# Kernel tuning notes

Hardware: AMD Instinct MI355X
Metric: run time of the kernel (lower is better)

Reference implementation:

```python
import jax, jax.numpy as jnp
import numpy as np
import math

PHI = (1.0 + math.sqrt(5.0)) / 2.0
LN_EPS = 1e-5


def _carrier_phases(n_heads: int) -> np.ndarray:
    """Reproduce DimensionalHeadManager._allocate carrier phases."""
    base = [k * math.pi / 7.0 for k in range(7)]  # rung base phases
    n_rungs = 7
    raw = []
    remaining = n_heads
    for i in range(n_rungs):
        if i < n_rungs - 1:
            c = max(1, round(n_heads / PHI ** (i + 1)))
            c = min(c, remaining - (n_rungs - 1 - i))
            raw.append(c)
            remaining -= c
        else:
            raw.append(max(1, remaining))
    phases = []
    for rung_idx, count in enumerate(raw):
        for j in range(count):
            phases.append(base[rung_idx] + 2.0 * math.pi / max(count, 1) * j)
    return np.asarray(phases[:n_heads], dtype=np.float32)


def setup_inputs() -> dict:
    key = jax.random.key(0)
    ks = jax.random.split(key, 7)
    B, S, D, H = 2, 2048, 1024, 16
    w_scale = 0.02  # realistic init scale for Linear weights
    x = jax.random.normal(ks[0], (B, S, D), dtype=jnp.float32)
    Wq = jax.random.normal(ks[1], (D, D), dtype=jnp.float32) * w_scale
    Wk = jax.random.normal(ks[2], (D, D), dtype=jnp.float32) * w_scale
    Wv = jax.random.normal(ks[3], (D, D), dtype=jnp.float32) * w_scale
    Wo = jax.random.normal(ks[4], (D, D), dtype=jnp.float32) * w_scale
    Wp = jax.random.normal(ks[5], (D,), dtype=jnp.float32) * w_scale  # W_phase (1,D) flattened
    gamma = jnp.ones((D,), dtype=jnp.float32)
    beta = jnp.zeros((D,), dtype=jnp.float32)
    carrier = jnp.asarray(_carrier_phases(H))  # srl.carrier_freq init
    lam = jnp.float32(0.1)  # lambda_resonance init
    return {"x": x, "Wq": Wq, "Wk": Wk, "Wv": Wv, "Wo": Wo, "Wp": Wp,
            "gamma": gamma, "beta": beta, "carrier": carrier, "lam": lam}


def reference(x, Wq, Wk, Wv, Wo, Wp, gamma, beta, carrier, lam):
    B, S, D = x.shape
    H = carrier.shape[0]
    dh = D // H
    scale = 1.0 / math.sqrt(dh)

    residual = x
    # LayerNorm
    mu = jnp.mean(x, axis=-1, keepdims=True)
    var = jnp.mean((x - mu) ** 2, axis=-1, keepdims=True)
    xn = (x - mu) * jax.lax.rsqrt(var + LN_EPS) * gamma + beta

    # Q/K/V projections (torch Linear: y = x @ W.T), split into heads
    q = jnp.einsum('bsd,ed->bse', xn, Wq).reshape(B, S, H, dh)
    k = jnp.einsum('bsd,ed->bse', xn, Wk).reshape(B, S, H, dh)
    v = jnp.einsum('bsd,ed->bse', xn, Wv).reshape(B, S, H, dh)

    # scalar phase per token, per-head carrier resonance gate
    phase = jnp.einsum('bsd,d->bs', xn, Wp)                       # (B,S)
    head_T = jnp.cos((phase[..., None] - carrier) * 0.5) ** 2     # (B,S,H)

    # attention scores + resonance term R_ij = cos^2((phi_i - phi_j)/2)
    scores = jnp.einsum('bihd,bjhd->bhij', q, k) * scale          # (B,H,S,S)
    R = jnp.cos((phase[:, :, None] - phase[:, None, :]) * 0.5) ** 2  # (B,S,S)
    scores = scores + lam * R[:, None, :, :]

    attn = jax.nn.softmax(scores, axis=-1)
    out = jnp.einsum('bhij,bjhd->bihd', attn, v)                  # (B,S,H,dh)
    out = out * head_T[..., None]                                 # per-head resonance gating
    emergent_energy = jnp.sum(jnp.abs(out))
    y = residual + jnp.einsum('bse,de->bsd', out.reshape(B, S, D), Wo)
    return (y, emergent_energy)
```

## Files before the change

kernel.cpp:

```cpp
#include <hip/hip_runtime.h>
#include <hip/hip_bf16.h>

#define S_LEN 2048
#define D_MODEL 1024
#define NH 16
#define DH 64
#define M_TOK 4096
#define DK 80

typedef __attribute__((ext_vector_type(8))) short bf16x8;
typedef __attribute__((ext_vector_type(4))) float f32x4;
typedef __attribute__((ext_vector_type(16))) float f32x16;

#define LOG2E 1.4426950408889634f

__device__ __forceinline__ unsigned short f2bf(float f) {
  unsigned u = __float_as_uint(f);
  u += 0x7FFF + ((u >> 16) & 1);
  return (unsigned short)(u >> 16);
}

__device__ __forceinline__ void gl16(const void* g, void* l) {
  __builtin_amdgcn_global_load_lds(
      (const __attribute__((address_space(1))) unsigned int*)g,
      (__attribute__((address_space(3))) unsigned int*)l, 16, 0, 0);
}

__global__ __launch_bounds__(256) void prep_kernel(
    const float* __restrict__ Wq, const float* __restrict__ Wk,
    const float* __restrict__ Wv, const float* __restrict__ Wo,
    unsigned short* __restrict__ wbf, float* __restrict__ energy) {
  if (blockIdx.x == 0 && threadIdx.x == 0) *energy = 0.f;
  int idx = (blockIdx.x * 256 + threadIdx.x) * 4;
  int wsel = idx >> 20;
  const float* s = (wsel == 0) ? Wq : (wsel == 1) ? Wk : (wsel == 2) ? Wv : Wo;
  int off = idx & 1048575;
  float4 v = *(const float4*)(s + off);
  ushort4 p;
  p.x = f2bf(v.x); p.y = f2bf(v.y); p.z = f2bf(v.z); p.w = f2bf(v.w);
  *(ushort4*)(wbf + idx) = p;
}

__device__ __forceinline__ float block_sum(float v, float* sm) {
#pragma unroll
  for (int o = 32; o > 0; o >>= 1) v += __shfl_xor(v, o, 64);
  int w = threadIdx.x >> 6;
  __syncthreads();
  if ((threadIdx.x & 63) == 0) sm[w] = v;
  __syncthreads();
  return sm[0] + sm[1] + sm[2] + sm[3];
}

__global__ __launch_bounds__(256) void ln_phase_kernel(
    const float* __restrict__ x, const float* __restrict__ Wp,
    const float* __restrict__ gamma, const float* __restrict__ beta,
    unsigned short* __restrict__ xn, float* __restrict__ cosP,
    float* __restrict__ sinP) {
  __shared__ float sm[4];
  int row = blockIdx.x;
  int tid = threadIdx.x;
  float4 v = ((const float4*)(x + (size_t)row * D_MODEL))[tid];
  float mu = block_sum(v.x + v.y + v.z + v.w, sm) * (1.0f / D_MODEL);
  float d0 = v.x - mu, d1 = v.y - mu, d2 = v.z - mu, d3 = v.w - mu;
  float var = block_sum(d0 * d0 + d1 * d1 + d2 * d2 + d3 * d3, sm) * (1.0f / D_MODEL);
  float rinv = rsqrtf(var + 1e-5f);
  float4 g = ((const float4*)gamma)[tid];
  float4 be = ((const float4*)beta)[tid];
  float n0 = d0 * rinv * g.x + be.x;
  float n1 = d1 * rinv * g.y + be.y;
  float n2 = d2 * rinv * g.z + be.z;
  float n3 = d3 * rinv * g.w + be.w;
  ushort4 p;
  p.x = f2bf(n0); p.y = f2bf(n1); p.z = f2bf(n2); p.w = f2bf(n3);
  ((ushort4*)(xn + (size_t)row * D_MODEL))[tid] = p;
  float4 wp = ((const float4*)Wp)[tid];
  float ph = block_sum(n0 * wp.x + n1 * wp.y + n2 * wp.z + n3 * wp.w, sm);
  if (tid == 0) {
    cosP[row] = cosf(ph);
    sinP[row] = sinf(ph);
  }
}

__global__ __launch_bounds__(256) void phase_fill_kernel(
    const float* __restrict__ cosP, const float* __restrict__ sinP,
    unsigned short* __restrict__ kk80) {
  int gid = blockIdx.x * 256 + threadIdx.x;
  int s = gid & (S_LEN - 1);
  int bh = gid >> 11;
  int b = bh >> 4;
  int tok = b * S_LEN + s;
  unsigned int w0 = (unsigned int)f2bf(cosP[tok]) | ((unsigned int)f2bf(sinP[tok]) << 16);
  *(int4*)(kk80 + (size_t)gid * DK + 64) = make_int4((int)w0, 0, 0, 0);
}

__global__ __launch_bounds__(256, 3) void qkv_gemm_kernel(
    const unsigned short* __restrict__ xn, const unsigned short* __restrict__ wbf,
    unsigned short* __restrict__ q, unsigned short* __restrict__ kk80,
    unsigned short* __restrict__ vT) {
  __shared__ __align__(16) unsigned short As[128 * 64];
  __shared__ __align__(16) unsigned short Bs[128 * 64];
  int bid = blockIdx.x;
  bool vmode = bid >= 512;
  const unsigned short* Ap;
  const unsigned short* Bp;
  int m0, n0;
  if (!vmode) {
    m0 = (bid >> 4) * 128;
    n0 = (bid & 15) * 128;
    Ap = xn; Bp = wbf;
  } else {
    int v2 = bid - 512;
    m0 = (v2 & 7) * 128;
    n0 = (v2 >> 3) * 128;
    Ap = wbf + 2 * D_MODEL * D_MODEL; Bp = xn;
  }
  int tid = threadIdx.x;
  int wave = tid >> 6, lane = tid & 63, quad = lane >> 4, l15 = lane & 15;
  int wm = (wave & 1) * 64, wn = (wave >> 1) * 64;
  f32x4 acc[4][4];
#pragma unroll
  for (int r = 0; r < 4; ++r)
#pragma unroll
    for (int c = 0; c < 4; ++c) acc[r][c] = (f32x4){0.f, 0.f, 0.f, 0.f};

  for (int k0 = 0; k0 < D_MODEL; k0 += 64) {
    __syncthreads();
#pragma unroll
    for (int t = 0; t < 4; ++t) {
      int c = t * 256 + tid;
      int r = c >> 3, p = c & 7;
      int g = p ^ (r & 7);
      gl16(&Ap[(size_t)(m0 + r) * D_MODEL + k0 + g * 8], &As[c * 8]);
      gl16(&Bp[(size_t)(n0 + r) * D_MODEL + k0 + g * 8], &Bs[c * 8]);
    }
    __syncthreads();
    bf16x8 af[4][2], bfr[4][2];
#pragma unroll
    for (int r = 0; r < 4; ++r) {
      int R = wm + r * 16 + l15;
#pragma unroll
      for (int h = 0; h < 2; ++h)
        af[r][h] = *(const bf16x8*)&As[R * 64 + ((h * 4 + quad) ^ (R & 7)) * 8];
    }
#pragma unroll
    for (int c = 0; c < 4; ++c) {
      int R = wn + c * 16 + l15;
#pragma unroll
      for (int h = 0; h < 2; ++h)
        bfr[c][h] = *(const bf16x8*)&Bs[R * 64 + ((h * 4 + quad) ^ (R & 7)) * 8];
    }
#pragma unroll
    for (int h = 0; h < 2; ++h)
#pragma unroll
      for (int r = 0; r < 4; ++r)
#pragma unroll
        for (int c = 0; c < 4; ++c)
          acc[r][c] = __builtin_amdgcn_mfma_f32_16x16x32_bf16(af[r][h], bfr[c][h], acc[r][c], 0, 0, 0);
  }
#pragma unroll
  for (int r = 0; r < 4; ++r) {
#pragma unroll
    for (int c = 0; c < 4; ++c) {
#pragma unroll
      for (int rr = 0; rr < 4; ++rr) {
        if (vmode) {
          int e = m0 + wm + r * 16 + quad * 4 + rr;
          int tok = n0 + wn + c * 16 + l15;
          int hh = e >> 6, d = e & 63;
          int bb = tok >> 11, ss = tok & (S_LEN - 1);
          vT[(((size_t)(bb * NH + hh)) * DH + d) * S_LEN + ss] = f2bf(acc[r][c][rr]);
        } else {
          int tok = m0 + wm + r * 16 + quad * 4 + rr;
          int n = n0 + wn + c * 16 + l15;
          int e = n & 1023;
          int hh = e >> 6, d = e & 63;
          int bb = tok >> 11, ss = tok & (S_LEN - 1);
          if ((n0 >> 10) == 0) {
            q[(((size_t)(bb * NH + hh)) * S_LEN + ss) * DH + d] =
                f2bf(acc[r][c][rr] * (0.125f * LOG2E));
          } else {
            kk80[(((size_t)(bb * NH + hh)) * S_LEN + ss) * DK + d] = f2bf(acc[r][c][rr]);
          }
        }
      }
    }
  }
}

__global__ __launch_bounds__(128, 3) void attn_kernel(
    const unsigned short* __restrict__ q, const unsigned short* __restrict__ kk80,
    const unsigned short* __restrict__ vT, const float* __restrict__ cosP,
    const float* __restrict__ sinP, const float* __restrict__ carrier,
    const float* __restrict__ lamp, unsigned short* __restrict__ outw,
    float* __restrict__ energy) {
  __shared__ __align__(16) unsigned short Ks[64 * 72];
  __shared__ __align__(16) unsigned short Vs[512 * 8];
  __shared__ __align__(16) unsigned int Ps[2][32 * 34];
  __shared__ float Lr[2][32];
  __shared__ float er[2];
  int qt = blockIdx.x, h = blockIdx.y, b = blockIdx.z;
  int bh = b * NH + h;
  int tid = threadIdx.x, wave = tid >> 6, lane = tid & 63;
  int half = lane >> 5, l31 = lane & 31;

  const unsigned short* kb = kk80 + (size_t)bh * S_LEN * DK;
  const unsigned short* vb = vT + (size_t)bh * DH * S_LEN;
  int qrow = qt * 64 + wave * 32 + l31;

  bf16x8 bQ[5];
  {
    const unsigned short* qp = q + ((size_t)bh * S_LEN + qrow) * DH;
#pragma unroll
    for (int db = 0; db < 4; ++db)
      bQ[db] = *(const bf16x8*)(qp + db * 16 + half * 8);
    bf16x8 z8 = {0, 0, 0, 0, 0, 0, 0, 0};
    if (half == 0) {
      float hl2 = 0.5f * lamp[0] * LOG2E;
      z8[0] = (short)f2bf(hl2 * cosP[b * S_LEN + qrow]);
      z8[1] = (short)f2bf(hl2 * sinP[b * S_LEN + qrow]);
    }
    bQ[4] = z8;
  }

  f32x16 O0 = {}, O1 = {};
  float l_i = 0.f;

  for (int j0 = 0; j0 < S_LEN; j0 += 64) {
    __syncthreads();
#pragma unroll
    for (int t = 0; t < 4; ++t) {
      unsigned int cc = t * 128 + tid;
      unsigned int r = cc / 9u, p = cc - r * 9u;
      gl16(&kb[(size_t)(j0 + r) * DK + p * 8], (unsigned short*)Ks + cc * 8);
    }
    if (tid < 64) {
      unsigned int cc = 512 + tid;
      unsigned int r = cc / 9u, p = cc - r * 9u;
      gl16(&kb[(size_t)(j0 + r) * DK + p * 8], (unsigned short*)Ks + cc * 8);
    }
#pragma unroll
    for (int t = 0; t < 4; ++t) {
      int cc = t * 128 + tid;
      int r = cc >> 3, p = cc & 7;
      int g = p ^ (r & 7);
      gl16(&vb[(size_t)r * S_LEN + j0 + g * 8], (unsigned short*)Vs + cc * 8);
    }
    __syncthreads();

    f32x16 Sf[2];
#pragma unroll
    for (int sj = 0; sj < 2; ++sj) {
      Sf[sj] = (f32x16){};
      int r = sj * 32 + l31;
#pragma unroll
      for (int db = 0; db < 5; ++db) {
        int p = (db < 4) ? (db * 2 + half) : 8;
        bf16x8 aK = *(const bf16x8*)((const unsigned short*)Ks + (r * 9 + p) * 8);
        Sf[sj] = __builtin_amdgcn_mfma_f32_32x32x16_bf16(aK, bQ[db], Sf[sj], 0, 0, 0);
      }
    }

#pragma unroll
    for (int sj = 0; sj < 2; ++sj) {
#pragma unroll
      for (int rr = 0; rr < 8; ++rr) {
        float e0 = exp2f(Sf[sj][rr * 2 + 0]);
        float e1 = exp2f(Sf[sj][rr * 2 + 1]);
        l_i += e0 + e1;
        __hip_bfloat162 pk = __float22bfloat162_rn(float2{e0, e1});
        int jd = sj * 16 + (rr >> 1) * 4 + half * 2 + (rr & 1);
        Ps[wave][l31 * 34 + jd] = *(unsigned int*)&pk;
      }
    }

#pragma unroll
    for (int jb = 0; jb < 4; ++jb) {
      const unsigned int* pp = &Ps[wave][l31 * 34 + jb * 8 + half * 4];
      uint2 a0 = *(const uint2*)pp;
      uint2 a1 = *(const uint2*)(pp + 2);
      union { unsigned int u[4]; bf16x8 v; } cvt;
      cvt.u[0] = a0.x; cvt.u[1] = a0.y; cvt.u[2] = a1.x; cvt.u[3] = a1.y;
      {
        int rv = l31;
        int p = (jb * 2 + half) ^ (rv & 7);
        bf16x8 bV = *(const bf16x8*)((const unsigned short*)Vs + (rv * 8 + p) * 8);
        O0 = __builtin_amdgcn_mfma_f32_32x32x16_bf16(cvt.v, bV, O0, 0, 0, 0);
      }
      {
        int rv = 32 + l31;
        int p = (jb * 2 + half) ^ (rv & 7);
        bf16x8 bV = *(const bf16x8*)((const unsigned short*)Vs + (rv * 8 + p) * 8);
        O1 = __builtin_amdgcn_mfma_f32_32x32x16_bf16(cvt.v, bV, O1, 0, 0, 0);
      }
    }
  }

  l_i += __shfl_xor(l_i, 32, 64);
  Lr[wave][l31] = l_i;
  float ch = cosf(carrier[h]), sh = sinf(carrier[h]);
  float esum = 0.f;
#pragma unroll
  for (int reg = 0; reg < 16; ++reg) {
    int ir = (reg & 3) + 8 * (reg >> 2) + 4 * half;
    int srow = qt * 64 + wave * 32 + ir;
    float cp = cosP[b * S_LEN + srow], sp = sinP[b * S_LEN + srow];
    float gate = 0.5f + 0.5f * (cp * ch + sp * sh);
    float gl = gate / Lr[wave][ir];
    float v0 = O0[reg] * gl, v1 = O1[reg] * gl;
    esum += fabsf(v0) + fabsf(v1);
    size_t tok = (size_t)b * S_LEN + srow;
    outw[tok * D_MODEL + h * DH + l31] = f2bf(v0);
    outw[tok * D_MODEL + h * DH + 32 + l31] = f2bf(v1);
  }
#pragma unroll
  for (int off = 32; off > 0; off >>= 1) esum += __shfl_xor(esum, off, 64);
  if (lane == 0) er[wave] = esum;
  __syncthreads();
  if (tid == 0) atomicAdd(energy, er[0] + er[1]);
}

__global__ __launch_bounds__(256) void out_gemm_kernel(
    const unsigned short* __restrict__ A, const unsigned short* __restrict__ Wo,
    const float* __restrict__ x, float* __restrict__ y) {
  __shared__ __align__(16) unsigned short As[128 * 64];
  __shared__ __align__(16) unsigned short Bs[64 * 64];
  int tid = threadIdx.x;
  int wave = tid >> 6, lane = tid & 63, quad = lane >> 4, l15 = lane & 15;
  int wm = (wave & 1) * 64, wn = (wave >> 1) * 32;
  int m0 = blockIdx.y * 128, n0 = blockIdx.x * 64;
  f32x4 acc[4][2];
#pragma unroll
  for (int r = 0; r < 4; ++r)
#pragma unroll
    for (int c = 0; c < 2; ++c) acc[r][c] = (f32x4){0.f, 0.f, 0.f, 0.f};

  for (int k0 = 0; k0 < D_MODEL; k0 += 64) {
    __syncthreads();
#pragma unroll
    for (int t = 0; t < 4; ++t) {
      int c = t * 256 + tid;
      int r = c >> 3, p = c & 7;
      int qc = p ^ (r & 7);
      gl16(&A[(size_t)(m0 + r) * D_MODEL + k0 + qc * 8], &As[c * 8]);
    }
#pragma unroll
    for (int t = 0; t < 2; ++t) {
      int c = t * 256 + tid;
      int r = c >> 3, p = c & 7;
      int qc = p ^ (r & 7);
      gl16(&Wo[(size_t)(n0 + r) * D_MODEL + k0 + qc * 8], &Bs[c * 8]);
    }
    __syncthreads();
    bf16x8 af[4][2], bfr[2][2];
#pragma unroll
    for (int r = 0; r < 4; ++r) {
      int R = wm + r * 16 + l15;
#pragma unroll
      for (int h = 0; h < 2; ++h)
        af[r][h] = *(const bf16x8*)&As[R * 64 + ((h * 4 + quad) ^ (R & 7)) * 8];
    }
#pragma unroll
    for (int c = 0; c < 2; ++c) {
      int R = wn + c * 16 + l15;
#pragma unroll
      for (int h = 0; h < 2; ++h)
        bfr[c][h] = *(const bf16x8*)&Bs[R * 64 + ((h * 4 + quad) ^ (R & 7)) * 8];
    }
#pragma unroll
    for (int h = 0; h < 2; ++h)
#pragma unroll
      for (int r = 0; r < 4; ++r)
#pragma unroll
        for (int c = 0; c < 2; ++c)
          acc[r][c] = __builtin_amdgcn_mfma_f32_16x16x32_bf16(af[r][h], bfr[c][h], acc[r][c], 0, 0, 0);
  }
#pragma unroll
  for (int r = 0; r < 4; ++r) {
#pragma unroll
    for (int c = 0; c < 2; ++c) {
      int dcol = n0 + wn + c * 16 + l15;
#pragma unroll
      for (int rr = 0; rr < 4; ++rr) {
        int tok = m0 + wm + r * 16 + quad * 4 + rr;
        size_t idx = (size_t)tok * D_MODEL + dcol;
        y[idx] = x[idx] + acc[r][c][rr];
      }
    }
  }
}

extern "C" void kernel_launch(void* const* d_in, const int* in_sizes, int n_in,
                              void* d_out, int out_size, void* d_ws, size_t ws_size,
                              hipStream_t stream) {
  const float* x = (const float*)d_in[0];
  const float* Wq = (const float*)d_in[1];
  const float* Wk = (const float*)d_in[2];
  const float* Wv = (const float*)d_in[3];
  const float* Wo = (const float*)d_in[4];
  const float* Wp = (const float*)d_in[5];
  const float* gamma = (const float*)d_in[6];
  const float* beta = (const float*)d_in[7];
  const float* carrier = (const float*)d_in[8];
  const float* lam = (const float*)d_in[9];

  char* ws = (char*)d_ws;
  const size_t MB = 1024 * 1024;
  unsigned short* wbf = (unsigned short*)(ws);
  unsigned short* xn = (unsigned short*)(ws + 8 * MB);
  unsigned short* qq = (unsigned short*)(ws + 16 * MB);
  unsigned short* kk80 = (unsigned short*)(ws + 24 * MB);
  unsigned short* vT = (unsigned short*)(ws + 34 * MB);
  float* cosP = (float*)(ws + 42 * MB);
  float* sinP = (float*)(ws + 42 * MB + 16 * 1024);
  unsigned short* outw = xn;

  float* y = (float*)d_out;
  float* energy = y + (out_size - 1);

  prep_kernel<<<4096, 256, 0, stream>>>(Wq, Wk, Wv, Wo, wbf, energy);
  ln_phase_kernel<<<M_TOK, 256, 0, stream>>>(x, Wp, gamma, beta, xn, cosP, sinP);
  phase_fill_kernel<<<256, 256, 0, stream>>>(cosP, sinP, kk80);
  qkv_gemm_kernel<<<768, 256, 0, stream>>>(xn, wbf, qq, kk80, vT);
  attn_kernel<<<dim3(32, 16, 2), 128, 0, stream>>>(qq, kk80, vT, cosP, sinP,
                                                   carrier, lam, outw, energy);
  out_gemm_kernel<<<dim3(16, 32), 256, 0, stream>>>(outw, wbf + 3 * D_MODEL * D_MODEL,
                                                    x, y);
}
```

Before: 228.5 us.

## Split attention keys across blocks with atomic partial merge and 4-wave blocks

The attention kernel now splits the key range into two halves across the grid and uses 256-thread blocks covering 128 query rows. Each K/V tile staged in LDS is therefore shared by four waves instead of two. Unnormalized outputs and row sums go to fp32 workspace buffers via atomicAdd. A new merge kernel then applies the softmax normalization and the per-head gate, writes bf16 output and accumulates the energy sum. This removes per-wave K/V load overhead but adds a 16MB memset, atomic traffic and an extra kernel pass.

New measurement: 257.7 us. 1.13x slower.

```diff
diff --git a/kernel.cpp b/kernel.cpp
--- a/kernel.cpp
+++ b/kernel.cpp
@@ -187,25 +187,23 @@
   }
 }
 
-__global__ __launch_bounds__(128, 3) void attn_kernel(
+__global__ __launch_bounds__(256, 4) void attn_kernel(
     const unsigned short* __restrict__ q, const unsigned short* __restrict__ kk80,
     const unsigned short* __restrict__ vT, const float* __restrict__ cosP,
-    const float* __restrict__ sinP, const float* __restrict__ carrier,
-    const float* __restrict__ lamp, unsigned short* __restrict__ outw,
-    float* __restrict__ energy) {
+    const float* __restrict__ sinP, const float* __restrict__ lamp,
+    float* __restrict__ Opart, float* __restrict__ lpart) {
   __shared__ __align__(16) unsigned short Ks[64 * 72];
   __shared__ __align__(16) unsigned short Vs[512 * 8];
-  __shared__ __align__(16) unsigned int Ps[2][32 * 34];
-  __shared__ float Lr[2][32];
-  __shared__ float er[2];
-  int qt = blockIdx.x, h = blockIdx.y, b = blockIdx.z;
+  __shared__ __align__(16) unsigned int Ps[4][32 * 34];
+  int qt = blockIdx.x, h = blockIdx.y;
+  int jh = blockIdx.z >> 1, b = blockIdx.z & 1;
   int bh = b * NH + h;
   int tid = threadIdx.x, wave = tid >> 6, lane = tid & 63;
   int half = lane >> 5, l31 = lane & 31;
 
   const unsigned short* kb = kk80 + (size_t)bh * S_LEN * DK;
   const unsigned short* vb = vT + (size_t)bh * DH * S_LEN;
-  int qrow = qt * 64 + wave * 32 + l31;
+  int qrow = qt * 128 + wave * 32 + l31;
 
   bf16x8 bQ[5];
   {
@@ -225,11 +223,12 @@
   f32x16 O0 = {}, O1 = {};
   float l_i = 0.f;
 
-  for (int j0 = 0; j0 < S_LEN; j0 += 64) {
-    __syncthreads();
-#pragma unroll
-    for (int t = 0; t < 4; ++t) {
-      unsigned int cc = t * 128 + tid;
+  for (int jt = 0; jt < S_LEN / 2; jt += 64) {
+    int j0 = jh * (S_LEN / 2) + jt;
+    __syncthreads();
+#pragma unroll
+    for (int t = 0; t < 2; ++t) {
+      unsigned int cc = t * 256 + tid;
       unsigned int r = cc / 9u, p = cc - r * 9u;
       gl16(&kb[(size_t)(j0 + r) * DK + p * 8], (unsigned short*)Ks + cc * 8);
     }
@@ -239,8 +238,8 @@
       gl16(&kb[(size_t)(j0 + r) * DK + p * 8], (unsigned short*)Ks + cc * 8);
     }
 #pragma unroll
-    for (int t = 0; t < 4; ++t) {
-      int cc = t * 128 + tid;
+    for (int t = 0; t < 2; ++t) {
+      int cc = t * 256 + tid;
       int r = cc >> 3, p = cc & 7;
       int g = p ^ (r & 7);
       gl16(&vb[(size_t)r * S_LEN + j0 + g * 8], (unsigned short*)Vs + cc * 8);
@@ -296,27 +295,50 @@
   }
 
   l_i += __shfl_xor(l_i, 32, 64);
-  Lr[wave][l31] = l_i;
-  float ch = cosf(carrier[h]), sh = sinf(carrier[h]);
-  float esum = 0.f;
+  size_t rowbase = (size_t)bh * S_LEN + qt * 128 + wave * 32;
+  if (half == 0) atomicAdd(lpart + rowbase + l31, l_i);
+  float* opb = Opart + rowbase * 64;
 #pragma unroll
   for (int reg = 0; reg < 16; ++reg) {
     int ir = (reg & 3) + 8 * (reg >> 2) + 4 * half;
-    int srow = qt * 64 + wave * 32 + ir;
-    float cp = cosP[b * S_LEN + srow], sp = sinP[b * S_LEN + srow];
-    float gate = 0.5f + 0.5f * (cp * ch + sp * sh);
-    float gl = gate / Lr[wave][ir];
-    float v0 = O0[reg] * gl, v1 = O1[reg] * gl;
-    esum += fabsf(v0) + fabsf(v1);
-    size_t tok = (size_t)b * S_LEN + srow;
-    outw[tok * D_MODEL + h * DH + l31] = f2bf(v0);
-    outw[tok * D_MODEL + h * DH + 32 + l31] = f2bf(v1);
-  }
+    atomicAdd(opb + (size_t)ir * 64 + l31, O0[reg]);
+    atomicAdd(opb + (size_t)ir * 64 + 32 + l31, O1[reg]);
+  }
+}
+
+__global__ __launch_bounds__(256) void merge_kernel(
+    const float* __restrict__ Opart, const float* __restrict__ lpart,
+    const float* __restrict__ cosP, const float* __restrict__ sinP,
+    const float* __restrict__ carrier, unsigned short* __restrict__ outw,
+    float* __restrict__ energy) {
+  __shared__ float er[4];
+  int tid = threadIdx.x;
+  int row = blockIdx.x * 32 + (tid >> 3);
+  int c0 = (tid & 7) * 8;
+  int b = row >> 15, h = (row >> 11) & 15, srow = row & (S_LEN - 1);
+  float l = lpart[row];
+  float cp = cosP[b * S_LEN + srow], sp = sinP[b * S_LEN + srow];
+  float ch = cosf(carrier[h]), sh = sinf(carrier[h]);
+  float gl = (0.5f + 0.5f * (cp * ch + sp * sh)) / l;
+  const float* op = Opart + (size_t)row * 64 + c0;
+  float4 a = *(const float4*)op;
+  float4 bb = *(const float4*)(op + 4);
+  float v[8] = {a.x, a.y, a.z, a.w, bb.x, bb.y, bb.z, bb.w};
+  float esum = 0.f;
+  unsigned short ob[8];
+#pragma unroll
+  for (int i = 0; i < 8; ++i) {
+    float t = v[i] * gl;
+    esum += fabsf(t);
+    ob[i] = f2bf(t);
+  }
+  size_t tok = (size_t)b * S_LEN + srow;
+  *(int4*)(outw + tok * D_MODEL + h * DH + c0) = *(int4*)&ob[0];
 #pragma unroll
   for (int off = 32; off > 0; off >>= 1) esum += __shfl_xor(esum, off, 64);
-  if (lane == 0) er[wave] = esum;
+  if ((tid & 63) == 0) er[tid >> 6] = esum;
   __syncthreads();
-  if (tid == 0) atomicAdd(energy, er[0] + er[1]);
+  if (tid == 0) atomicAdd(energy, er[0] + er[1] + er[2] + er[3]);
 }
 
 __global__ __launch_bounds__(256) void out_gemm_kernel(
@@ -412,6 +434,8 @@
   unsigned short* vT = (unsigned short*)(ws + 34 * MB);
   float* cosP = (float*)(ws + 42 * MB);
   float* sinP = (float*)(ws + 42 * MB + 16 * 1024);
+  float* Opart = (float*)(ws + 43 * MB);
+  float* lpart = (float*)(ws + 59 * MB);
   unsigned short* outw = xn;
 
   float* y = (float*)d_out;
@@ -420,9 +444,12 @@
   prep_kernel<<<4096, 256, 0, stream>>>(Wq, Wk, Wv, Wo, wbf, energy);
   ln_phase_kernel<<<M_TOK, 256, 0, stream>>>(x, Wp, gamma, beta, xn, cosP, sinP);
   phase_fill_kernel<<<256, 256, 0, stream>>>(cosP, sinP, kk80);
+  hipMemsetAsync(ws + 43 * MB, 0, 16 * MB + 256 * 1024, stream);
   qkv_gemm_kernel<<<768, 256, 0, stream>>>(xn, wbf, qq, kk80, vT);
-  attn_kernel<<<dim3(32, 16, 2), 128, 0, stream>>>(qq, kk80, vT, cosP, sinP,
-                                                   carrier, lam, outw, energy);
+  attn_kernel<<<dim3(16, 16, 4), 256, 0, stream>>>(qq, kk80, vT, cosP, sinP,
+                                                   lam, Opart, lpart);
+  merge_kernel<<<2048, 256, 0, stream>>>(Opart, lpart, cosP, sinP, carrier,
+                                         outw, energy);
   out_gemm_kernel<<<dim3(16, 32), 256, 0, stream>>>(outw, wbf + 3 * D_MODEL * D_MODEL,
                                                     x, y);
 }
```

## Stage QKV epilogue through LDS, fuse phase fill into LN, remap attention blocks per XCD

Applied to the files above, without the earlier changes.

The QKV GEMM epilogue now writes accumulators to a padded shared-memory tile and then emits coalesced 128-byte row stores, replacing scattered 2-byte stores to q, kk80 and vT. The separate phase_fill kernel is folded into the LayerNorm kernel, removing one launch and a reread of cosP/sinP. The attention grid is flattened to 1D and remapped so that each XCD handles four contiguous (batch, head) pairs, which is meant to improve K/V L2 reuse. The costs are a larger LDS footprint and an extra sync in the GEMM epilogue.

Result: no change. 232.8 us (+1.9%).

```diff
diff --git a/kernel.cpp b/kernel.cpp
--- a/kernel.cpp
+++ b/kernel.cpp
@@ -55,7 +55,7 @@
     const float* __restrict__ x, const float* __restrict__ Wp,
     const float* __restrict__ gamma, const float* __restrict__ beta,
     unsigned short* __restrict__ xn, float* __restrict__ cosP,
-    float* __restrict__ sinP) {
+    float* __restrict__ sinP, unsigned short* __restrict__ kk80) {
   __shared__ float sm[4];
   int row = blockIdx.x;
   int tid = threadIdx.x;
@@ -75,30 +75,26 @@
   ((ushort4*)(xn + (size_t)row * D_MODEL))[tid] = p;
   float4 wp = ((const float4*)Wp)[tid];
   float ph = block_sum(n0 * wp.x + n1 * wp.y + n2 * wp.z + n3 * wp.w, sm);
-  if (tid == 0) {
-    cosP[row] = cosf(ph);
-    sinP[row] = sinf(ph);
-  }
-}
-
-__global__ __launch_bounds__(256) void phase_fill_kernel(
-    const float* __restrict__ cosP, const float* __restrict__ sinP,
-    unsigned short* __restrict__ kk80) {
-  int gid = blockIdx.x * 256 + threadIdx.x;
-  int s = gid & (S_LEN - 1);
-  int bh = gid >> 11;
-  int b = bh >> 4;
-  int tok = b * S_LEN + s;
-  unsigned int w0 = (unsigned int)f2bf(cosP[tok]) | ((unsigned int)f2bf(sinP[tok]) << 16);
-  *(int4*)(kk80 + (size_t)gid * DK + 64) = make_int4((int)w0, 0, 0, 0);
+  if (tid < 16) {
+    float cp = cosf(ph), sp = sinf(ph);
+    if (tid == 0) {
+      cosP[row] = cp;
+      sinP[row] = sp;
+    }
+    int b = row >> 11, s = row & (S_LEN - 1);
+    unsigned int w0 = (unsigned int)f2bf(cp) | ((unsigned int)f2bf(sp) << 16);
+    size_t gid = (size_t)(b * NH + tid) * S_LEN + s;
+    *(int4*)(kk80 + gid * DK + 64) = make_int4((int)w0, 0, 0, 0);
+  }
 }
 
 __global__ __launch_bounds__(256, 3) void qkv_gemm_kernel(
     const unsigned short* __restrict__ xn, const unsigned short* __restrict__ wbf,
     unsigned short* __restrict__ q, unsigned short* __restrict__ kk80,
     unsigned short* __restrict__ vT) {
-  __shared__ __align__(16) unsigned short As[128 * 64];
-  __shared__ __align__(16) unsigned short Bs[128 * 64];
+  __shared__ __align__(16) unsigned short Sm[128 * 136];
+  unsigned short* As = Sm;
+  unsigned short* Bs = Sm + 128 * 64;
   int bid = blockIdx.x;
   bool vmode = bid >= 512;
   const unsigned short* Ap;
@@ -157,34 +153,43 @@
         for (int c = 0; c < 4; ++c)
           acc[r][c] = __builtin_amdgcn_mfma_f32_16x16x32_bf16(af[r][h], bfr[c][h], acc[r][c], 0, 0, 0);
   }
-#pragma unroll
-  for (int r = 0; r < 4; ++r) {
-#pragma unroll
-    for (int c = 0; c < 4; ++c) {
+  __syncthreads();
+  float scl = (!vmode && n0 < 1024) ? (0.125f * LOG2E) : 1.0f;
+#pragma unroll
+  for (int r = 0; r < 4; ++r)
+#pragma unroll
+    for (int c = 0; c < 4; ++c)
 #pragma unroll
       for (int rr = 0; rr < 4; ++rr) {
-        if (vmode) {
-          int e = m0 + wm + r * 16 + quad * 4 + rr;
-          int tok = n0 + wn + c * 16 + l15;
-          int hh = e >> 6, d = e & 63;
-          int bb = tok >> 11, ss = tok & (S_LEN - 1);
-          vT[(((size_t)(bb * NH + hh)) * DH + d) * S_LEN + ss] = f2bf(acc[r][c][rr]);
-        } else {
-          int tok = m0 + wm + r * 16 + quad * 4 + rr;
-          int n = n0 + wn + c * 16 + l15;
-          int e = n & 1023;
-          int hh = e >> 6, d = e & 63;
-          int bb = tok >> 11, ss = tok & (S_LEN - 1);
-          if ((n0 >> 10) == 0) {
-            q[(((size_t)(bb * NH + hh)) * S_LEN + ss) * DH + d] =
-                f2bf(acc[r][c][rr] * (0.125f * LOG2E));
-          } else {
-            kk80[(((size_t)(bb * NH + hh)) * S_LEN + ss) * DK + d] = f2bf(acc[r][c][rr]);
-          }
-        }
-      }
-    }
-  }
+        int m = wm + r * 16 + quad * 4 + rr;
+        int n = wn + c * 16 + l15;
+        Sm[m * 136 + n] = f2bf(acc[r][c][rr] * scl);
+      }
+  __syncthreads();
+  int r2 = tid >> 1, h64 = (tid & 1) * 64;
+  const unsigned short* src = &Sm[r2 * 136 + h64];
+  unsigned short* dst;
+  if (!vmode) {
+    int tok = m0 + r2;
+    int bb = tok >> 11, ss = tok & (S_LEN - 1);
+    int n = n0 + h64;
+    if (n < 1024) {
+      int hh = n >> 6;
+      dst = q + (((size_t)(bb * NH + hh)) * S_LEN + ss) * DH;
+    } else {
+      int hh = (n >> 6) & 15;
+      dst = kk80 + (((size_t)(bb * NH + hh)) * S_LEN + ss) * DK;
+    }
+  } else {
+    int e = m0 + r2;
+    int hh = e >> 6, d = e & 63;
+    int tok = n0 + h64;
+    int bb = tok >> 11, ss = tok & (S_LEN - 1);
+    dst = vT + (((size_t)(bb * NH + hh)) * DH + d) * S_LEN + ss;
+  }
+#pragma unroll
+  for (int i = 0; i < 8; ++i)
+    *(int4*)(dst + i * 8) = *(const int4*)(src + i * 8);
 }
 
 __global__ __launch_bounds__(128, 3) void attn_kernel(
@@ -198,8 +203,11 @@
   __shared__ __align__(16) unsigned int Ps[2][32 * 34];
   __shared__ float Lr[2][32];
   __shared__ float er[2];
-  int qt = blockIdx.x, h = blockIdx.y, b = blockIdx.z;
-  int bh = b * NH + h;
+  int bid = blockIdx.x;
+  int xcd = bid & 7, g = bid >> 3;
+  int bh = xcd * 4 + (g >> 5);
+  int qt = g & 31;
+  int b = bh >> 4, h = bh & 15;
   int tid = threadIdx.x, wave = tid >> 6, lane = tid & 63;
   int half = lane >> 5, l31 = lane & 31;
 
@@ -242,8 +250,8 @@
     for (int t = 0; t < 4; ++t) {
       int cc = t * 128 + tid;
       int r = cc >> 3, p = cc & 7;
-      int g = p ^ (r & 7);
-      gl16(&vb[(size_t)r * S_LEN + j0 + g * 8], (unsigned short*)Vs + cc * 8);
+      int g2 = p ^ (r & 7);
+      gl16(&vb[(size_t)r * S_LEN + j0 + g2 * 8], (unsigned short*)Vs + cc * 8);
     }
     __syncthreads();
 
@@ -418,11 +426,11 @@
   float* energy = y + (out_size - 1);
 
   prep_kernel<<<4096, 256, 0, stream>>>(Wq, Wk, Wv, Wo, wbf, energy);
-  ln_phase_kernel<<<M_TOK, 256, 0, stream>>>(x, Wp, gamma, beta, xn, cosP, sinP);
-  phase_fill_kernel<<<256, 256, 0, stream>>>(cosP, sinP, kk80);
+  ln_phase_kernel<<<M_TOK, 256, 0, stream>>>(x, Wp, gamma, beta, xn, cosP, sinP,
+                                             kk80);
   qkv_gemm_kernel<<<768, 256, 0, stream>>>(xn, wbf, qq, kk80, vT);
-  attn_kernel<<<dim3(32, 16, 2), 128, 0, stream>>>(qq, kk80, vT, cosP, sinP,
-                                                   carrier, lam, outw, energy);
+  attn_kernel<<<1024, 128, 0, stream>>>(qq, kk80, vT, cosP, sinP, carrier, lam,
+                                        outw, energy);
   out_gemm_kernel<<<dim3(16, 32), 256, 0, stream>>>(outw, wbf + 3 * D_MODEL * D_MODEL,
                                                     x, y);
 }
```
